# Optimization experiments

Measured on AMD Instinct MI355X. Metric: run time of the kernel, lower is better.

Reference implementation:

```python
import jax, jax.numpy as jnp
from jax import lax
import numpy as np

N = 10000      # nodes
T = 60         # lookback window
F = 16         # features per timestep
HL = 256       # lstm hidden dim
GH = 8         # gat heads
GC = 64        # gat out channels per head
GD = GH * GC   # 512 concat dim
FH = 512       # fusion hidden
E = 320000     # edges (before self loops)


def _lstm_layer(x, w_ih, w_hh, b_ih, b_hh):
    # x: [T, N, in] -> hidden sequence [T, N, HL]; torch gate order i,f,g,o
    n = x.shape[1]
    h0 = jnp.zeros((n, HL), x.dtype)
    def step(carry, xt):
        h, c = carry
        g = xt @ w_ih.T + h @ w_hh.T + b_ih + b_hh
        i, f, gg, o = jnp.split(g, 4, axis=-1)
        c = jax.nn.sigmoid(f) * c + jax.nn.sigmoid(i) * jnp.tanh(gg)
        h = jax.nn.sigmoid(o) * jnp.tanh(c)
        return (h, c), h
    _, hs = lax.scan(step, (h0, h0), x)
    return hs


def _gatv2(x, src, dst, ea, wl, bl, wr, br, we, att, bias):
    # GATv2Conv (concat=True, edge_dim=1, negative_slope=0.2); self loops already in src/dst/ea
    n = x.shape[0]
    xl = (x @ wl + bl).reshape(n, GH, GC)   # lin_l (source / x_j)
    xr = (x @ wr + br).reshape(n, GH, GC)   # lin_r (target / x_i)
    ee = (ea @ we).reshape(-1, GH, GC)      # lin_edge (bias=False)
    m = jax.nn.leaky_relu(xl[src] + xr[dst] + ee, 0.2)      # [E', GH, GC]
    logits = jnp.einsum('ehc,hc->eh', m, att)               # [E', GH]
    mx = jax.ops.segment_max(logits, dst, num_segments=n)
    ex = jnp.exp(logits - mx[dst])
    den = jax.ops.segment_sum(ex, dst, num_segments=n)
    alpha = ex / den[dst]                                   # softmax over in-edges per node
    out = jax.ops.segment_sum(xl[src] * alpha[..., None], dst, num_segments=n)
    return out.reshape(n, GD) + bias


def setup_inputs():
    key = jax.random.key(0)
    ks = jax.random.split(key, 20)
    f32 = jnp.float32
    def nrm(k, shp, fan):
        return jax.random.normal(k, shp, f32) * (1.0 / np.sqrt(fan))
    return {
        "x_seq": jax.random.normal(ks[0], (N, T, F), f32),
        "edge_index": jax.random.randint(ks[1], (2, E), 0, N, jnp.int32),
        "edge_attr": jax.random.uniform(ks[2], (E, 1), dtype=f32),
        "w_ih0": nrm(ks[3], (4 * HL, F), HL), "w_hh0": nrm(ks[4], (4 * HL, HL), HL),
        "b_ih0": jnp.zeros((4 * HL,), f32), "b_hh0": jnp.zeros((4 * HL,), f32),
        "w_ih1": nrm(ks[5], (4 * HL, HL), HL), "w_hh1": nrm(ks[6], (4 * HL, HL), HL),
        "b_ih1": jnp.zeros((4 * HL,), f32), "b_hh1": jnp.zeros((4 * HL,), f32),
        "g0_wl": nrm(ks[7], (HL, GD), HL), "g0_bl": jnp.zeros((GD,), f32),
        "g0_wr": nrm(ks[8], (HL, GD), HL), "g0_br": jnp.zeros((GD,), f32),
        "g0_we": nrm(ks[9], (1, GD), 1),
        "g0_att": nrm(ks[10], (GH, GC), GC), "g0_bias": jnp.zeros((GD,), f32),
        "g1_wl": nrm(ks[11], (GD, GD), GD), "g1_bl": jnp.zeros((GD,), f32),
        "g1_wr": nrm(ks[12], (GD, GD), GD), "g1_br": jnp.zeros((GD,), f32),
        "g1_we": nrm(ks[13], (1, GD), 1),
        "g1_att": nrm(ks[14], (GH, GC), GC), "g1_bias": jnp.zeros((GD,), f32),
        "fc1_w": nrm(ks[15], (HL + GD, FH), HL + GD), "fc1_b": jnp.zeros((FH,), f32),
        "fc2_w": nrm(ks[16], (FH, 1), FH), "fc2_b": jnp.zeros((1,), f32),
    }


def reference(x_seq, edge_index, edge_attr,
              w_ih0, w_hh0, b_ih0, b_hh0, w_ih1, w_hh1, b_ih1, b_hh1,
              g0_wl, g0_bl, g0_wr, g0_br, g0_we, g0_att, g0_bias,
              g1_wl, g1_bl, g1_wr, g1_br, g1_we, g1_att, g1_bias,
              fc1_w, fc1_b, fc2_w, fc2_b):
    # 2-layer LSTM encoder, take last timestep hidden (dropout off: eval mode)
    xt = jnp.transpose(x_seq, (1, 0, 2))            # [T, N, F]
    h1 = _lstm_layer(xt, w_ih0, w_hh0, b_ih0, b_hh0)
    h2 = _lstm_layer(h1, w_ih1, w_hh1, b_ih1, b_hh1)
    node = h2[-1]                                    # [N, HL]
    # add self loops; fill edge_attr for loops with mean (PyG default fill_value='mean')
    loop = jnp.arange(N, dtype=edge_index.dtype)
    src = jnp.concatenate([edge_index[0], loop])
    dst = jnp.concatenate([edge_index[1], loop])
    ea = jnp.concatenate([edge_attr, jnp.broadcast_to(edge_attr.mean(axis=0), (N, 1))], axis=0)
    g = jax.nn.elu(_gatv2(node, src, dst, ea, g0_wl, g0_bl, g0_wr, g0_br, g0_we, g0_att, g0_bias))
    g = jax.nn.elu(_gatv2(g, src, dst, ea, g1_wl, g1_bl, g1_wr, g1_br, g1_we, g1_att, g1_bias))
    fused = jnp.concatenate([node, g], axis=1)       # [N, HL+GD]
    h = jax.nn.relu(fused @ fc1_w + fc1_b)
    return h @ fc2_w + fc2_b                         # [N, 1]
```

## Files before the change

kernel.cpp:

```cpp
#include <hip/hip_runtime.h>

#define DEV __device__ __forceinline__

typedef _Float16 f16;
typedef _Float16 f16x8 __attribute__((ext_vector_type(8)));
typedef _Float16 f16x2 __attribute__((ext_vector_type(2)));
typedef float f32x4 __attribute__((ext_vector_type(4)));

DEV float sigmoidf_(float x) { return 1.0f / (1.0f + __expf(-x)); }
DEV float tanhf2_(float x)   { return 1.0f - 2.0f / (__expf(2.0f * x) + 1.0f); }

DEV void load_lds16(const void* g, void* l) {
    __builtin_amdgcn_global_load_lds(
        (const __attribute__((address_space(1))) char*)(const char*)g,
        (__attribute__((address_space(3))) char*)(unsigned int)(unsigned long long)(char*)l,
        16, 0, 0);
}

DEV int swz(int row, int ck) { return ck ^ (row & 3) ^ ((row >> 2) & 3); }

__global__ void prep_w0_kernel(const float* __restrict__ wih,
                               const float* __restrict__ whh,
                               f16* __restrict__ dst) {
    int idx = blockIdx.x * 256 + threadIdx.x;
    if (idx >= 1024 * 288) return;
    int rd = idx / 288, k = idx - rd * 288;
    int T = rd >> 7, p = rd & 127;
    int u = T * 32 + ((p >> 6) & 1) * 16 + (p & 15);
    int g = (p >> 4) & 3;
    int src = g * 256 + u;
    float v;
    if (k < 16)        v = wih[src * 16 + k];
    else if (k < 272)  v = whh[src * 256 + (k - 16)];
    else               v = 0.f;
    dst[idx] = (f16)v;
}

__global__ void prep_w1_kernel(const float* __restrict__ wih,
                               const float* __restrict__ whh,
                               f16* __restrict__ dst) {
    int idx = blockIdx.x * 256 + threadIdx.x;
    if (idx >= 1024 * 512) return;
    int rd = idx >> 9, k = idx & 511;
    int T = rd >> 7, p = rd & 127;
    int u = T * 32 + ((p >> 6) & 1) * 16 + (p & 15);
    int g = (p >> 4) & 3;
    int src = g * 256 + u;
    float v = (k < 256) ? wih[src * 256 + k] : whh[src * 256 + (k - 256)];
    dst[idx] = (f16)v;
}

__global__ void prep_bias4_kernel(const float* __restrict__ bi,
                                  const float* __restrict__ bh,
                                  float* __restrict__ dst) {
    int idx = blockIdx.x * 256 + threadIdx.x;
    if (idx >= 1024) return;
    int u = idx >> 2, g = idx & 3;
    dst[idx] = bi[g * 256 + u] + bh[g * 256 + u];
}

__global__ void prep_wt_kernel(const float* __restrict__ src, f16* __restrict__ dst,
                               int K, int N) {
    int idx = blockIdx.x * 256 + threadIdx.x;
    if (idx >= K * N) return;
    int n = idx / K, k = idx - n * K;
    dst[idx] = (f16)src[(size_t)k * N + n];
}

__global__ void prep_x0_kernel(const float* __restrict__ x_seq, f16* __restrict__ A0,
                               int Nn) {
    int idx = blockIdx.x * 256 + threadIdx.x;
    if (idx >= Nn * 16) return;
    int m = idx >> 4, f = idx & 15;
    A0[(size_t)m * 288 + f] = (f16)x_seq[(size_t)m * 960 + f];
}

DEV void tile_load_chunk(const f16* __restrict__ A, int lda,
                         const f16* __restrict__ Bt, int K,
                         int m0, int n0, int k0,
                         f16* __restrict__ sA, f16* __restrict__ sB,
                         int w, int arow, int achk)
{
#pragma unroll
    for (int c = 0; c < 2; ++c) {
        int R = c * 64 + w * 16;
        load_lds16(A + (size_t)(m0 + R + arow) * lda + k0 + achk, sA + R * 32);
        load_lds16(Bt + (size_t)(n0 + R + arow) * K + k0 + achk, sB + R * 32);
    }
}

DEV void tile_compute_chunk(const f16* __restrict__ sA, const f16* __restrict__ sB,
                            f32x4 (&acc)[4][4], int wr, int wc, int frow, int fsl)
{
    f16x8 af[4], bf[4];
#pragma unroll
    for (int i = 0; i < 4; ++i)
        af[i] = *(const f16x8*)&sA[(wr + i * 16 + frow) * 32 + fsl];
#pragma unroll
    for (int j = 0; j < 4; ++j)
        bf[j] = *(const f16x8*)&sB[(wc + j * 16 + frow) * 32 + fsl];
#pragma unroll
    for (int i = 0; i < 4; ++i)
#pragma unroll
        for (int j = 0; j < 4; ++j)
            acc[i][j] = __builtin_amdgcn_mfma_f32_16x16x32_f16(af[i], bf[j], acc[i][j], 0, 0, 0);
}

DEV void gemm_tile_lds(const f16* __restrict__ A, int lda,
                       const f16* __restrict__ Bt, int K,
                       int m0, int n0,
                       f16* __restrict__ sA, f16* __restrict__ sB,
                       f32x4 (&acc)[4][4])
{
    const int tid = threadIdx.x;
    const int w = tid >> 6, lane = tid & 63;
    const int arow = lane >> 2;
    const int achk = swz(arow, lane & 3) * 8;
    const int frow = lane & 15, l4 = lane >> 4;
    const int fsl = swz(frow, l4) * 8;
    const int wr = (w >> 1) * 64, wc = (w & 1) * 64;
    const int nch = K >> 5;

    tile_load_chunk(A, lda, Bt, K, m0, n0, 0, sA, sB, w, arow, achk);
    if (nch > 1)
        tile_load_chunk(A, lda, Bt, K, m0, n0, 32, sA + 4096, sB + 4096, w, arow, achk);

    int cb = 0, lb = 2;
    for (int kc = 0; kc < nch; ++kc) {
        if (kc + 1 < nch) asm volatile("s_waitcnt vmcnt(4)" ::: "memory");
        else              asm volatile("s_waitcnt vmcnt(0)" ::: "memory");
        __builtin_amdgcn_s_barrier();
        if (kc + 2 < nch)
            tile_load_chunk(A, lda, Bt, K, m0, n0, (kc + 2) * 32,
                            sA + lb * 4096, sB + lb * 4096, w, arow, achk);
        tile_compute_chunk(sA + cb * 4096, sB + cb * 4096, acc, wr, wc, frow, fsl);
        cb = (cb == 2) ? 0 : cb + 1;
        lb = (lb == 2) ? 0 : lb + 1;
    }
}

DEV void lstm_step_core(
    f16* __restrict__ sA, f16* __restrict__ sB,
    int bx, int by,
    const f16* __restrict__ A, int lda, int K,
    const f16* __restrict__ Wt,
    const float* __restrict__ bias4,
    float* __restrict__ c_state,
    f16* __restrict__ hA, int ldhA, int offhA,
    f16* __restrict__ hB, int ldhB, int offhB,
    const float* __restrict__ xsrc, int tnext,
    int M)
{
    const int tid = threadIdx.x;
    const int w = tid >> 6, lane = tid & 63;
    const int m0 = bx * 128, n0 = by * 128;
    const int wr = (w >> 1) * 64;

    const int u = by * 32 + (w & 1) * 16 + (lane & 15);
    const int rbase = m0 + wr + (lane >> 4) * 4;
    float cold[4][4];
#pragma unroll
    for (int i = 0; i < 4; ++i)
#pragma unroll
        for (int r = 0; r < 4; ++r)
            cold[i][r] = c_state[(size_t)(rbase + i * 16 + r) * 256 + u];

    f32x4 acc[4][4] = {};
    gemm_tile_lds(A, lda, Wt, K, m0, n0, sA, sB, acc);

    const float4 bb = *(const float4*)&bias4[u * 4];
#pragma unroll
    for (int i = 0; i < 4; ++i) {
#pragma unroll
        for (int r = 0; r < 4; ++r) {
            int m = rbase + i * 16 + r;
            if (m < M) {
                float gi = sigmoidf_(acc[i][0][r] + bb.x);
                float gf = sigmoidf_(acc[i][1][r] + bb.y);
                float gg = tanhf2_(acc[i][2][r] + bb.z);
                float go = sigmoidf_(acc[i][3][r] + bb.w);
                float cn = gf * cold[i][r] + gi * gg;
                c_state[(size_t)m * 256 + u] = cn;
                f16 h = (f16)(go * tanhf2_(cn));
                hA[(size_t)m * ldhA + offhA + u] = h;
                if (hB) hB[(size_t)m * ldhB + offhB + u] = h;
            }
        }
    }
    if (xsrc && by == 0) {
        int row = tid >> 1, fb = (tid & 1) * 8;
        int m = m0 + row;
        if (m < M) {
            const float* xp = xsrc + (size_t)m * 960 + tnext * 16 + fb;
            f16* dp = hB + (size_t)m * ldhB + fb;
#pragma unroll
            for (int q = 0; q < 8; ++q) dp[q] = (f16)xp[q];
        }
    }
}

__global__ __launch_bounds__(256) void lstm_mfma_kernel(
    const f16* __restrict__ A, int lda, int K,
    const f16* __restrict__ Wt, const float* __restrict__ bias4,
    float* __restrict__ c_state,
    f16* __restrict__ hA, int ldhA, int offhA,
    f16* __restrict__ hB, int ldhB, int offhB,
    const float* __restrict__ xsrc, int tnext, int M, int mtiles)
{
    __shared__ __align__(16) f16 sA[3 * 4096];
    __shared__ __align__(16) f16 sB[3 * 4096];
    const int l = blockIdx.x;
    const int xcd = l & 7, q = l >> 3;
    const int y = q & 7, xhi = q >> 3;
    const int x = xhi * 8 + xcd;
    if (x >= mtiles) return;
    lstm_step_core(sA, sB, x, y, A, lda, K, Wt, bias4, c_state,
                   hA, ldhA, offhA, hB, ldhB, offhB, xsrc, tnext, M);
}

__global__ __launch_bounds__(256) void lstm_dual_kernel(
    const f16* __restrict__ A1, const f16* __restrict__ W1t,
    const float* __restrict__ b41, float* __restrict__ c1,
    f16* __restrict__ h1A, int ldh1A, int offh1A,
    const f16* __restrict__ A0, const f16* __restrict__ W0t,
    const float* __restrict__ b40, float* __restrict__ c0,
    f16* __restrict__ h0A, int ldh0A, int offh0A,
    f16* __restrict__ h0B, int ldh0B, int offh0B,
    const float* __restrict__ xsrc, int tnext, int M, int mtiles)
{
    __shared__ __align__(16) f16 sA[3 * 4096];
    __shared__ __align__(16) f16 sB[3 * 4096];
    const int l = blockIdx.x;
    const int xcd = l & 7, q = l >> 3;
    const int yz = q & 15, xhi = q >> 4;
    const int x = xhi * 8 + xcd;
    if (x >= mtiles) return;
    const int y = yz & 7, z = yz >> 3;
    if (z == 0)
        lstm_step_core(sA, sB, x, y, A1, 512, 512, W1t, b41, c1,
                       h1A, ldh1A, offh1A, nullptr, 0, 0, nullptr, 0, M);
    else
        lstm_step_core(sA, sB, x, y, A0, 288, 288, W0t, b40, c0,
                       h0A, ldh0A, offh0A, h0B, ldh0B, offh0B, xsrc, tnext, M);
}

__global__ __launch_bounds__(256) void gemm16_kernel(
    const f16* __restrict__ A, int lda,
    const f16* __restrict__ Bt, int K,
    const float* __restrict__ bias,
    f16* __restrict__ C16, float* __restrict__ C32, int ldc,
    int act, int M)
{
    __shared__ __align__(16) f16 sA[3 * 4096];
    __shared__ __align__(16) f16 sB[3 * 4096];
    const int tid = threadIdx.x;
    const int w = tid >> 6, lane = tid & 63;
    const int m0 = blockIdx.x * 128, n0 = blockIdx.y * 128;
    const int wr = (w >> 1) * 64, wcn = (w & 1) * 64;

    f32x4 acc[4][4] = {};
    gemm_tile_lds(A, lda, Bt, K, m0, n0, sA, sB, acc);

    const int rbase = m0 + wr + (lane >> 4) * 4;
#pragma unroll
    for (int i = 0; i < 4; ++i) {
#pragma unroll
        for (int r = 0; r < 4; ++r) {
            int m = rbase + i * 16 + r;
            if (m >= M) continue;
#pragma unroll
            for (int j = 0; j < 4; ++j) {
                int n = n0 + wcn + j * 16 + (lane & 15);
                float v = acc[i][j][r] + bias[n];
                if (act == 1) v = fmaxf(v, 0.f);
                if (C16) C16[(size_t)m * ldc + n] = (f16)v;
                else     C32[(size_t)m * ldc + n] = v;
            }
        }
    }
}

__global__ __launch_bounds__(256) void gemm16_dual_kernel(
    const f16* __restrict__ A, int lda,
    const f16* __restrict__ Btl, const f16* __restrict__ Btr, int K,
    const float* __restrict__ biasl, const float* __restrict__ biasr,
    f16* __restrict__ Cl, f16* __restrict__ Cr, int ldc, int M)
{
    __shared__ __align__(16) f16 sA[3 * 4096];
    __shared__ __align__(16) f16 sB[3 * 4096];
    const int side = blockIdx.y >> 2;
    const f16* Bt = side ? Btr : Btl;
    const float* bias = side ? biasr : biasl;
    f16* C16 = side ? Cr : Cl;
    const int tid = threadIdx.x;
    const int w = tid >> 6, lane = tid & 63;
    const int m0 = blockIdx.x * 128, n0 = (blockIdx.y & 3) * 128;
    const int wr = (w >> 1) * 64, wcn = (w & 1) * 64;

    f32x4 acc[4][4] = {};
    gemm_tile_lds(A, lda, Bt, K, m0, n0, sA, sB, acc);

    const int rbase = m0 + wr + (lane >> 4) * 4;
#pragma unroll
    for (int i = 0; i < 4; ++i) {
#pragma unroll
        for (int r = 0; r < 4; ++r) {
            int m = rbase + i * 16 + r;
            if (m >= M) continue;
#pragma unroll
            for (int j = 0; j < 4; ++j) {
                int n = n0 + wcn + j * 16 + (lane & 15);
                float v = acc[i][j][r] + bias[n];
                C16[(size_t)m * ldc + n] = (f16)v;
            }
        }
    }
}

__global__ void mean_sum_kernel(const float* __restrict__ a, int n, float* __restrict__ out) {
    __shared__ float s[256];
    float loc = 0.f;
    for (int i = blockIdx.x * 256 + threadIdx.x; i < n; i += gridDim.x * 256) loc += a[i];
    s[threadIdx.x] = loc;
    __syncthreads();
    for (int off = 128; off; off >>= 1) {
        if (threadIdx.x < off) s[threadIdx.x] += s[threadIdx.x + off];
        __syncthreads();
    }
    if (threadIdx.x == 0) atomicAdd(out, s[0]);
}

__global__ void hist_kernel(const int* __restrict__ ei, int Ne, int Nn,
                            int* __restrict__ counts) {
    int e = blockIdx.x * 256 + threadIdx.x;
    if (e >= Ne + Nn) return;
    int d = (e < Ne) ? ei[Ne + e] : (e - Ne);
    atomicAdd(&counts[d], 1);
}

__global__ void scan_kernel(const int* __restrict__ counts, int* __restrict__ offsets, int n) {
    __shared__ int s[256];
    int tid = threadIdx.x;
    int chunk = (n + 255) / 256;
    int b = tid * chunk;
    int loc = 0;
    for (int j = 0; j < chunk; ++j) { int i = b + j; if (i < n) loc += counts[i]; }
    s[tid] = loc;
    __syncthreads();
    for (int off = 1; off < 256; off <<= 1) {
        int v = (tid >= off) ? s[tid - off] : 0;
        __syncthreads();
        s[tid] += v;
        __syncthreads();
    }
    int run = (tid == 0) ? 0 : s[tid - 1];
    for (int j = 0; j < chunk; ++j) {
        int i = b + j;
        if (i < n) { offsets[i] = run; run += counts[i]; }
    }
    if (tid == 255) offsets[n] = run;
}

__global__ void scatter_kernel(const int* __restrict__ ei, const float* __restrict__ ea,
                               const float* __restrict__ sump, float inv_ne, int Ne, int Nn,
                               int* __restrict__ cursor, int* __restrict__ src_sorted,
                               float* __restrict__ ea_sorted) {
    int e = blockIdx.x * 256 + threadIdx.x;
    if (e >= Ne + Nn) return;
    int s, d; float a;
    if (e < Ne) { s = ei[e]; d = ei[Ne + e]; a = ea[e]; }
    else        { s = e - Ne; d = s; a = sump[0] * inv_ne; }
    int pos = atomicAdd(&cursor[d], 1);
    src_sorted[pos] = s;
    ea_sorted[pos] = a;
}

__global__ __launch_bounds__(256) void gat_fused_kernel(
    const f16* __restrict__ xl, const f16* __restrict__ xr,
    const float* __restrict__ we, const float* __restrict__ att,
    const float* __restrict__ bias,
    const int* __restrict__ offsets, const int* __restrict__ src_sorted,
    const float* __restrict__ ea_sorted,
    f16* __restrict__ out, int ldo, int N)
{
    __shared__ float s_acc[8][4][64];
    __shared__ float s_m[4][64];
    __shared__ float s_den[4][64];
    const int i = blockIdx.x;
    const int tid = threadIdx.x;
    const int w = tid >> 6, lane = tid & 63;
    const int c8 = lane * 8;

    f16x8 xrv = *(const f16x8*)&xr[(size_t)i * 512 + c8];
    float xr_[8], we_[8], at_[8];
#pragma unroll
    for (int k = 0; k < 8; ++k) xr_[k] = (float)xrv[k];
    *(float4*)&we_[0] = *(const float4*)&we[c8];
    *(float4*)&we_[4] = *(const float4*)&we[c8 + 4];
    *(float4*)&at_[0] = *(const float4*)&att[c8];
    *(float4*)&at_[4] = *(const float4*)&att[c8 + 4];

    const int beg = offsets[i], end = offsets[i + 1];

    float m = -1e30f, den = 0.f;
    float acc[8] = {};

    int e = beg + w;
    float a_c = 0.f, a_n = 0.f;
    f16x8 xv_c = {}, xv_n = {};
    if (e < end) {
        a_c = ea_sorted[e];
        xv_c = *(const f16x8*)&xl[(size_t)src_sorted[e] * 512 + c8];
    }
    if (e + 4 < end) {
        a_n = ea_sorted[e + 4];
        xv_n = *(const f16x8*)&xl[(size_t)src_sorted[e + 4] * 512 + c8];
    }
    for (; e < end; e += 4) {
        float a = a_c; f16x8 xv = xv_c;
        a_c = a_n; xv_c = xv_n;
        if (e + 8 < end) {
            int sn = src_sorted[e + 8];
            a_n = ea_sorted[e + 8];
            xv_n = *(const f16x8*)&xl[(size_t)sn * 512 + c8];
        }
        float x[8];
        float p = 0.f;
#pragma unroll
        for (int k = 0; k < 8; ++k) {
            x[k] = (float)xv[k];
            float v = x[k] + xr_[k] + a * we_[k];
            v = (v > 0.f) ? v : 0.2f * v;
            p = fmaf(v, at_[k], p);
        }
        p += __shfl_xor(p, 1);
        p += __shfl_xor(p, 2);
        p += __shfl_xor(p, 4);
        if (__all(p <= m + 8.f)) {
            float wg = __expf(p - m);
            den += wg;
#pragma unroll
            for (int k = 0; k < 8; ++k) acc[k] = fmaf(wg, x[k], acc[k]);
        } else {
            float mn = fmaxf(m, p);
            float r  = __expf(m - mn);
            float wg = __expf(p - mn);
            den = den * r + wg;
#pragma unroll
            for (int k = 0; k < 8; ++k) acc[k] = fmaf(acc[k], r, wg * x[k]);
            m = mn;
        }
    }

    s_m[w][lane] = m;
    s_den[w][lane] = den;
#pragma unroll
    for (int k = 0; k < 8; ++k) s_acc[k][w][lane] = acc[k];
    __syncthreads();

    const int c2 = tid * 2;
    const int l = c2 >> 3;
    const int k0 = c2 & 7;
    float m0 = s_m[0][l], m1 = s_m[1][l], m2 = s_m[2][l], m3 = s_m[3][l];
    float M = fmaxf(fmaxf(m0, m1), fmaxf(m2, m3));
    float e0 = __expf(m0 - M), e1 = __expf(m1 - M);
    float e2 = __expf(m2 - M), e3 = __expf(m3 - M);
    float D = s_den[0][l] * e0 + s_den[1][l] * e1 + s_den[2][l] * e2 + s_den[3][l] * e3;
    float A0 = s_acc[k0][0][l] * e0 + s_acc[k0][1][l] * e1
             + s_acc[k0][2][l] * e2 + s_acc[k0][3][l] * e3;
    float A1 = s_acc[k0 + 1][0][l] * e0 + s_acc[k0 + 1][1][l] * e1
             + s_acc[k0 + 1][2][l] * e2 + s_acc[k0 + 1][3][l] * e3;
    float rD = 1.f / D;
    float v0 = A0 * rD + bias[c2];
    float v1 = A1 * rD + bias[c2 + 1];
    v0 = (v0 > 0.f) ? v0 : __expf(v0) - 1.f;
    v1 = (v1 > 0.f) ? v1 : __expf(v1) - 1.f;
    f16x2 ov; ov.x = (f16)v0; ov.y = (f16)v1;
    *(f16x2*)&out[(size_t)i * ldo + c2] = ov;
}

__global__ void fc2_kernel(const float* __restrict__ H, const float* __restrict__ w,
                           const float* __restrict__ b, float* __restrict__ out, int N) {
    int wv = threadIdx.x >> 6, lane = threadIdx.x & 63;
    int node = blockIdx.x * 4 + wv;
    if (node >= N) return;
    float s = 0.f;
#pragma unroll
    for (int j = 0; j < 8; ++j)
        s += H[(size_t)node * 512 + j * 64 + lane] * w[j * 64 + lane];
#pragma unroll
    for (int off = 32; off; off >>= 1) s += __shfl_xor(s, off, 64);
    if (lane == 0) out[node] = s + b[0];
}

extern "C" void kernel_launch(void* const* d_in, const int* in_sizes, int n_in,
                              void* d_out, int out_size, void* d_ws, size_t ws_size,
                              hipStream_t stream) {
    const float* x_seq     = (const float*)d_in[0];
    const int*   edge_index= (const int*)d_in[1];
    const float* edge_attr = (const float*)d_in[2];
    const float* w_ih0 = (const float*)d_in[3];
    const float* w_hh0 = (const float*)d_in[4];
    const float* b_ih0 = (const float*)d_in[5];
    const float* b_hh0 = (const float*)d_in[6];
    const float* w_ih1 = (const float*)d_in[7];
    const float* w_hh1 = (const float*)d_in[8];
    const float* b_ih1 = (const float*)d_in[9];
    const float* b_hh1 = (const float*)d_in[10];
    const float* g0_wl = (const float*)d_in[11];
    const float* g0_bl = (const float*)d_in[12];
    const float* g0_wr = (const float*)d_in[13];
    const float* g0_br = (const float*)d_in[14];
    const float* g0_we = (const float*)d_in[15];
    const float* g0_att= (const float*)d_in[16];
    const float* g0_bias=(const float*)d_in[17];
    const float* g1_wl = (const float*)d_in[18];
    const float* g1_bl = (const float*)d_in[19];
    const float* g1_wr = (const float*)d_in[20];
    const float* g1_br = (const float*)d_in[21];
    const float* g1_we = (const float*)d_in[22];
    const float* g1_att= (const float*)d_in[23];
    const float* g1_bias=(const float*)d_in[24];
    const float* fc1_w = (const float*)d_in[25];
    const float* fc1_b = (const float*)d_in[26];
    const float* fc2_w = (const float*)d_in[27];
    const float* fc2_b = (const float*)d_in[28];
    float* out = (float*)d_out;

    const int Nn = in_sizes[0] / (60 * 16);
    const int Ne = in_sizes[1] / 2;
    const int Etot = Ne + Nn;
    const int MT = (Nn + 127) / 128;
    const int Mpad = MT * 128;
    const int MTpad8 = ((MT + 7) / 8) * 8;

    size_t off = 0;
    auto alloc = [&](size_t bytes) -> void* {
        void* r = (char*)d_ws + off;
        off += (bytes + 255) & ~(size_t)255;
        return r;
    };
    f16* W0t   = (f16*)alloc((size_t)1024 * 288 * 2);
    f16* W1t   = (f16*)alloc((size_t)1024 * 512 * 2);
    float* b40 = (float*)alloc(1024 * 4);
    float* b41 = (float*)alloc(1024 * 4);
    f16* Wg0l  = (f16*)alloc((size_t)512 * 256 * 2);
    f16* Wg0r  = (f16*)alloc((size_t)512 * 256 * 2);
    f16* Wg1l  = (f16*)alloc((size_t)512 * 512 * 2);
    f16* Wg1r  = (f16*)alloc((size_t)512 * 512 * 2);
    f16* Wfc1  = (f16*)alloc((size_t)512 * 768 * 2);
    f16* A0b[2]; A0b[0] = (f16*)alloc((size_t)Mpad * 288 * 2);
                 A0b[1] = (f16*)alloc((size_t)Mpad * 288 * 2);
    f16* A1b[2]; A1b[0] = (f16*)alloc((size_t)Mpad * 512 * 2);
                 A1b[1] = (f16*)alloc((size_t)Mpad * 512 * 2);
    float* c0  = (float*)alloc((size_t)Mpad * 256 * 4);
    float* c1  = (float*)alloc((size_t)Mpad * 256 * 4);
    f16* fused = (f16*)alloc((size_t)Mpad * 768 * 2);
    f16* xlbuf = (f16*)alloc((size_t)Mpad * 512 * 2);
    f16* xrbuf = (f16*)alloc((size_t)Mpad * 512 * 2);
    f16* gbuf  = (f16*)alloc((size_t)Mpad * 512 * 2);
    float* hfc1= (float*)alloc((size_t)Mpad * 512 * 4);
    int* counts  = (int*)alloc((size_t)Nn * 4);
    int* offsets = (int*)alloc((size_t)(Nn + 1) * 4);
    int* cursor  = (int*)alloc((size_t)Nn * 4);
    int* src_sorted = (int*)alloc((size_t)Etot * 4);
    float* ea_sorted = (float*)alloc((size_t)Etot * 4);
    float* meanp = (float*)alloc(256);

    prep_w0_kernel<<<dim3((1024 * 288 + 255) / 256), 256, 0, stream>>>(w_ih0, w_hh0, W0t);
    prep_w1_kernel<<<dim3((1024 * 512 + 255) / 256), 256, 0, stream>>>(w_ih1, w_hh1, W1t);
    prep_bias4_kernel<<<dim3(4), 256, 0, stream>>>(b_ih0, b_hh0, b40);
    prep_bias4_kernel<<<dim3(4), 256, 0, stream>>>(b_ih1, b_hh1, b41);
    prep_wt_kernel<<<dim3((256 * 512 + 255) / 256), 256, 0, stream>>>(g0_wl, Wg0l, 256, 512);
    prep_wt_kernel<<<dim3((256 * 512 + 255) / 256), 256, 0, stream>>>(g0_wr, Wg0r, 256, 512);
    prep_wt_kernel<<<dim3((512 * 512 + 255) / 256), 256, 0, stream>>>(g1_wl, Wg1l, 512, 512);
    prep_wt_kernel<<<dim3((512 * 512 + 255) / 256), 256, 0, stream>>>(g1_wr, Wg1r, 512, 512);
    prep_wt_kernel<<<dim3((768 * 512 + 255) / 256), 256, 0, stream>>>(fc1_w, Wfc1, 768, 512);
    hipMemsetAsync(A0b[0], 0, (size_t)Mpad * 288 * 2, stream);
    hipMemsetAsync(A0b[1], 0, (size_t)Mpad * 288 * 2, stream);
    hipMemsetAsync(A1b[0], 0, (size_t)Mpad * 512 * 2, stream);
    hipMemsetAsync(c0, 0, (size_t)Mpad * 256 * 4, stream);
    hipMemsetAsync(c1, 0, (size_t)Mpad * 256 * 4, stream);
    prep_x0_kernel<<<dim3((Nn * 16 + 255) / 256), 256, 0, stream>>>(x_seq, A0b[0], Nn);

    hipMemsetAsync(meanp, 0, 4, stream);
    hipMemsetAsync(counts, 0, (size_t)Nn * 4, stream);
    mean_sum_kernel<<<dim3(256), 256, 0, stream>>>(edge_attr, Ne, meanp);
    hist_kernel<<<dim3((Etot + 255) / 256), 256, 0, stream>>>(edge_index, Ne, Nn, counts);
    scan_kernel<<<dim3(1), 256, 0, stream>>>(counts, offsets, Nn);
    hipMemcpyAsync(cursor, offsets, (size_t)Nn * 4, hipMemcpyDeviceToDevice, stream);
    scatter_kernel<<<dim3((Etot + 255) / 256), 256, 0, stream>>>(
        edge_index, edge_attr, meanp, 1.0f / (float)Ne, Ne, Nn, cursor, src_sorted, ea_sorted);

    const int solo_grid = MTpad8 * 8;
    const int dual_grid = MTpad8 * 16;
    lstm_mfma_kernel<<<dim3(solo_grid), 256, 0, stream>>>(
        A0b[0], 288, 288, W0t, b40, c0,
        A1b[0], 512, 0,
        A0b[1], 288, 16,
        x_seq, 1, Nn, MT);
    for (int k = 0; k < 59; ++k) {
        lstm_dual_kernel<<<dim3(dual_grid), 256, 0, stream>>>(
            A1b[k & 1], W1t, b41, c1,
            A1b[(k + 1) & 1], 512, 256,
            A0b[(k + 1) & 1], W0t, b40, c0,
            A1b[(k + 1) & 1], 512, 0,
            A0b[k & 1], 288, 16,
            (k + 1 < 59) ? x_seq : nullptr, k + 2, Nn, MT);
    }
    lstm_mfma_kernel<<<dim3(solo_grid), 256, 0, stream>>>(
        A1b[1], 512, 512, W1t, b41, c1,
        fused, 768, 0,
        nullptr, 0, 0,
        nullptr, 0, Nn, MT);

    gemm16_dual_kernel<<<dim3(MT, 8), 256, 0, stream>>>(
        fused, 768, Wg0l, Wg0r, 256, g0_bl, g0_br, xlbuf, xrbuf, 512, Nn);
    gat_fused_kernel<<<dim3(Nn), 256, 0, stream>>>(
        xlbuf, xrbuf, g0_we, g0_att, g0_bias, offsets, src_sorted, ea_sorted,
        gbuf, 512, Nn);

    gemm16_dual_kernel<<<dim3(MT, 8), 256, 0, stream>>>(
        gbuf, 512, Wg1l, Wg1r, 512, g1_bl, g1_br, xlbuf, xrbuf, 512, Nn);
    gat_fused_kernel<<<dim3(Nn), 256, 0, stream>>>(
        xlbuf, xrbuf, g1_we, g1_att, g1_bias, offsets, src_sorted, ea_sorted,
        fused + 256, 768, Nn);

    gemm16_kernel<<<dim3(MT, 4), 256, 0, stream>>>(
        fused, 768, Wfc1, 768, fc1_b, nullptr, hfc1, 512, 1, Nn);
    fc2_kernel<<<dim3((Nn + 3) / 4), 256, 0, stream>>>(hfc1, fc2_w, fc2_b, out, Nn);
}
```

Measured before the change: 2.742 ms.

## Replace per-timestep LSTM launches with persistent cooperative kernel using grid sync

The 61 separate LSTM step launches are replaced by one cooperative persistent kernel of 768 blocks. Each block handles up to two fixed tiles and keeps its cell state in registers instead of global memory, with a grid-wide sync between timesteps. This removes launch overhead and the c_state round-trips. In exchange it depends on cooperative launch support and an occupancy of at least 3 blocks per CU, and some blocks run two tiles serially, which can unbalance each step.

```diff
diff --git a/kernel.cpp b/kernel.cpp
--- a/kernel.cpp
+++ b/kernel.cpp
@@ -1,4 +1,7 @@
 #include <hip/hip_runtime.h>
+#include <hip/hip_cooperative_groups.h>
+
+namespace cg = cooperative_groups;
 
 #define DEV __device__ __forceinline__
 
@@ -139,6 +142,128 @@
     }
 }
 
+DEV void lstm_tile_step(
+    f16* __restrict__ sA, f16* __restrict__ sB,
+    int bx, int by,
+    const f16* __restrict__ A, int lda, int K,
+    const f16* __restrict__ Wt,
+    const float* __restrict__ bias4,
+    float (&cst)[4][4],
+    f16* __restrict__ hA, int ldhA, int offhA,
+    f16* __restrict__ hB, int ldhB, int offhB,
+    const float* __restrict__ xsrc, int tnext,
+    int M)
+{
+    const int tid = threadIdx.x;
+    const int w = tid >> 6, lane = tid & 63;
+    const int m0 = bx * 128, n0 = by * 128;
+    const int wr = (w >> 1) * 64;
+    const int u = by * 32 + (w & 1) * 16 + (lane & 15);
+    const int rbase = m0 + wr + (lane >> 4) * 4;
+
+    f32x4 acc[4][4] = {};
+    gemm_tile_lds(A, lda, Wt, K, m0, n0, sA, sB, acc);
+
+    const float4 bb = *(const float4*)&bias4[u * 4];
+#pragma unroll
+    for (int i = 0; i < 4; ++i) {
+#pragma unroll
+        for (int r = 0; r < 4; ++r) {
+            int m = rbase + i * 16 + r;
+            if (m < M) {
+                float gi = sigmoidf_(acc[i][0][r] + bb.x);
+                float gf = sigmoidf_(acc[i][1][r] + bb.y);
+                float gg = tanhf2_(acc[i][2][r] + bb.z);
+                float go = sigmoidf_(acc[i][3][r] + bb.w);
+                float cn = gf * cst[i][r] + gi * gg;
+                cst[i][r] = cn;
+                f16 h = (f16)(go * tanhf2_(cn));
+                hA[(size_t)m * ldhA + offhA + u] = h;
+                if (hB) hB[(size_t)m * ldhB + offhB + u] = h;
+            }
+        }
+    }
+    if (xsrc && by == 0) {
+        int row = tid >> 1, fb = (tid & 1) * 8;
+        int m = m0 + row;
+        if (m < M) {
+            const float* xp = xsrc + (size_t)m * 960 + tnext * 16 + fb;
+            f16* dp = hB + (size_t)m * ldhB + fb;
+#pragma unroll
+            for (int q = 0; q < 8; ++q) dp[q] = (f16)xp[q];
+        }
+    }
+}
+
+DEV void persist_tile(
+    f16* __restrict__ sA, f16* __restrict__ sB,
+    int x, int y, int z, int t,
+    float (&cst)[4][4],
+    const f16* __restrict__ W1t, const float* __restrict__ b41,
+    const f16* __restrict__ W0t, const float* __restrict__ b40,
+    f16* __restrict__ A1b0, f16* __restrict__ A1b1,
+    f16* __restrict__ A0b0, f16* __restrict__ A0b1,
+    f16* __restrict__ fused, const float* __restrict__ x_seq,
+    int M, int mtiles)
+{
+    if (x >= mtiles) return;
+    if (z == 0) {
+        if (t < 1) return;
+        int tt = t - 1;
+        const f16* A = (tt & 1) ? A1b1 : A1b0;
+        f16* hA; int ldhA, offhA;
+        if (tt == 59) { hA = fused; ldhA = 768; offhA = 0; }
+        else { hA = ((tt + 1) & 1) ? A1b1 : A1b0; ldhA = 512; offhA = 256; }
+        lstm_tile_step(sA, sB, x, y, A, 512, 512, W1t, b41, cst,
+                       hA, ldhA, offhA, nullptr, 0, 0, nullptr, 0, M);
+    } else {
+        if (t > 59) return;
+        int tt = t;
+        const f16* A = (tt & 1) ? A0b1 : A0b0;
+        f16* hA = (tt & 1) ? A1b1 : A1b0;
+        f16* hB = ((tt + 1) & 1) ? A0b1 : A0b0;
+        lstm_tile_step(sA, sB, x, y, A, 288, 288, W0t, b40, cst,
+                       hA, 512, 0, hB, 288, 16,
+                       (tt < 59) ? x_seq : nullptr, tt + 1, M);
+    }
+}
+
+__global__ __launch_bounds__(256) void lstm_persist_kernel(
+    const f16* __restrict__ W1t, const float* __restrict__ b41,
+    const f16* __restrict__ W0t, const float* __restrict__ b40,
+    f16* __restrict__ A1b0, f16* __restrict__ A1b1,
+    f16* __restrict__ A0b0, f16* __restrict__ A0b1,
+    f16* __restrict__ fused, const float* __restrict__ x_seq,
+    int M, int mtiles, int nblk)
+{
+    __shared__ __align__(16) f16 sA[3 * 4096];
+    __shared__ __align__(16) f16 sB[3 * 4096];
+    cg::grid_group grid = cg::this_grid();
+
+    const int b = blockIdx.x;
+    int x1, y1, z1;
+    { int v = b; z1 = (v >= 640) ? 1 : 0; int i = v - z1 * 640;
+      int xcd = i & 7, q = i >> 3; y1 = q & 7; x1 = (q >> 3) * 8 + xcd; }
+    const int v2i = b + nblk;
+    const bool has2 = v2i < 1280;
+    int x2 = 0, y2 = 0, z2 = 0;
+    if (has2) { int v = v2i; z2 = (v >= 640) ? 1 : 0; int i = v - z2 * 640;
+                int xcd = i & 7, q = i >> 3; y2 = q & 7; x2 = (q >> 3) * 8 + xcd; }
+
+    float cT1[4][4] = {};
+    float cT2[4][4] = {};
+
+    for (int t = 0; t <= 60; ++t) {
+        persist_tile(sA, sB, x1, y1, z1, t, cT1, W1t, b41, W0t, b40,
+                     A1b0, A1b1, A0b0, A0b1, fused, x_seq, M, mtiles);
+        __syncthreads();
+        if (has2)
+            persist_tile(sA, sB, x2, y2, z2, t, cT2, W1t, b41, W0t, b40,
+                         A1b0, A1b1, A0b0, A0b1, fused, x_seq, M, mtiles);
+        if (t < 60) grid.sync();
+    }
+}
+
 DEV void lstm_step_core(
     f16* __restrict__ sA, f16* __restrict__ sB,
     int bx, int by,
@@ -153,9 +278,8 @@
 {
     const int tid = threadIdx.x;
     const int w = tid >> 6, lane = tid & 63;
-    const int m0 = bx * 128, n0 = by * 128;
+    const int m0 = bx * 128;
     const int wr = (w >> 1) * 64;
-
     const int u = by * 32 + (w & 1) * 16 + (lane & 15);
     const int rbase = m0 + wr + (lane >> 4) * 4;
     float cold[4][4];
@@ -166,7 +290,7 @@
             cold[i][r] = c_state[(size_t)(rbase + i * 16 + r) * 256 + u];
 
     f32x4 acc[4][4] = {};
-    gemm_tile_lds(A, lda, Wt, K, m0, n0, sA, sB, acc);
+    gemm_tile_lds(A, lda, Wt, K, m0, by * 128, sA, sB, acc);
 
     const float4 bb = *(const float4*)&bias4[u * 4];
 #pragma unroll
@@ -579,8 +703,7 @@
     hipMemsetAsync(A0b[0], 0, (size_t)Mpad * 288 * 2, stream);
     hipMemsetAsync(A0b[1], 0, (size_t)Mpad * 288 * 2, stream);
     hipMemsetAsync(A1b[0], 0, (size_t)Mpad * 512 * 2, stream);
-    hipMemsetAsync(c0, 0, (size_t)Mpad * 256 * 4, stream);
-    hipMemsetAsync(c1, 0, (size_t)Mpad * 256 * 4, stream);
+    hipMemsetAsync(A1b[1], 0, (size_t)Mpad * 512 * 2, stream);
     prep_x0_kernel<<<dim3((Nn * 16 + 255) / 256), 256, 0, stream>>>(x_seq, A0b[0], Nn);
 
     hipMemsetAsync(meanp, 0, 4, stream);
@@ -592,27 +715,55 @@
     scatter_kernel<<<dim3((Etot + 255) / 256), 256, 0, stream>>>(
         edge_index, edge_attr, meanp, 1.0f / (float)Ne, Ne, Nn, cursor, src_sorted, ea_sorted);
 
-    const int solo_grid = MTpad8 * 8;
-    const int dual_grid = MTpad8 * 16;
-    lstm_mfma_kernel<<<dim3(solo_grid), 256, 0, stream>>>(
-        A0b[0], 288, 288, W0t, b40, c0,
-        A1b[0], 512, 0,
-        A0b[1], 288, 16,
-        x_seq, 1, Nn, MT);
-    for (int k = 0; k < 59; ++k) {
-        lstm_dual_kernel<<<dim3(dual_grid), 256, 0, stream>>>(
-            A1b[k & 1], W1t, b41, c1,
-            A1b[(k + 1) & 1], 512, 256,
-            A0b[(k + 1) & 1], W0t, b40, c0,
-            A1b[(k + 1) & 1], 512, 0,
-            A0b[k & 1], 288, 16,
-            (k + 1 < 59) ? x_seq : nullptr, k + 2, Nn, MT);
-    }
-    lstm_mfma_kernel<<<dim3(solo_grid), 256, 0, stream>>>(
-        A1b[1], 512, 512, W1t, b41, c1,
-        fused, 768, 0,
-        nullptr, 0, 0,
-        nullptr, 0, Nn, MT);
+    int coopDone = 0;
+    {
+        int occ = 0;
+        hipError_t qe = hipOccupancyMaxActiveBlocksPerMultiprocessor(
+            &occ, lstm_persist_kernel, 256, 0);
+        if (qe == hipSuccess && occ >= 3) {
+            int nblk = 768;
+            f16* A1b0_ = A1b[0]; f16* A1b1_ = A1b[1];
+            f16* A0b0_ = A0b[0]; f16* A0b1_ = A0b[1];
+            f16* fused_ = fused;
+            const float* xs_ = x_seq;
+            int M_ = Nn, MT_ = MT, NB_ = nblk;
+            const f16* W1t_ = W1t; const float* b41_ = b41;
+            const f16* W0t_ = W0t; const float* b40_ = b40;
+            void* kargs[] = {
+                (void*)&W1t_, (void*)&b41_, (void*)&W0t_, (void*)&b40_,
+                (void*)&A1b0_, (void*)&A1b1_, (void*)&A0b0_, (void*)&A0b1_,
+                (void*)&fused_, (void*)&xs_, (void*)&M_, (void*)&MT_, (void*)&NB_
+            };
+            hipError_t le = hipLaunchCooperativeKernel(
+                lstm_persist_kernel, dim3(nblk), dim3(256), kargs, 0, stream);
+            if (le == hipSuccess) coopDone = 1;
+        }
+    }
+    if (!coopDone) {
+        hipMemsetAsync(c0, 0, (size_t)Mpad * 256 * 4, stream);
+        hipMemsetAsync(c1, 0, (size_t)Mpad * 256 * 4, stream);
+        const int solo_grid = MTpad8 * 8;
+        const int dual_grid = MTpad8 * 16;
+        lstm_mfma_kernel<<<dim3(solo_grid), 256, 0, stream>>>(
+            A0b[0], 288, 288, W0t, b40, c0,
+            A1b[0], 512, 0,
+            A0b[1], 288, 16,
+            x_seq, 1, Nn, MT);
+        for (int k = 0; k < 59; ++k) {
+            lstm_dual_kernel<<<dim3(dual_grid), 256, 0, stream>>>(
+                A1b[k & 1], W1t, b41, c1,
+                A1b[(k + 1) & 1], 512, 256,
+                A0b[(k + 1) & 1], W0t, b40, c0,
+                A1b[(k + 1) & 1], 512, 0,
+                A0b[k & 1], 288, 16,
+                (k + 1 < 59) ? x_seq : nullptr, k + 2, Nn, MT);
+        }
+        lstm_mfma_kernel<<<dim3(solo_grid), 256, 0, stream>>>(
+            A1b[1], 512, 512, W1t, b41, c1,
+            fused, 768, 0,
+            nullptr, 0, 0,
+            nullptr, 0, Nn, MT);
+    }
 
     gemm16_dual_kernel<<<dim3(MT, 8), 256, 0, stream>>>(
         fused, 768, Wg0l, Wg0r, 256, g0_bl, g0_br, xlbuf, xrbuf, 512, Nn);
```

Result: slower. 2.842 ms (+3.6%).
